# Kernel tuning notes

Hardware: AMD Instinct MI355X
Metric: run time of the kernel (lower is better)

The kernel has to match this reference:

```python
import jax, jax.numpy as jnp
import numpy as np

# bitsandbytes NF4 codebook (16 levels)
NF4 = jnp.array([-1.0, -0.6961928009986877, -0.5250730514526367, -0.39491748809814453,
                 -0.28444138169288635, -0.18477343022823334, -0.09105003625154495, 0.0,
                 0.07958029955625534, 0.16093020141124725, 0.24611230194568634,
                 0.33791524171829224, 0.44070982933044434, 0.5626170039176941,
                 0.7229568362236023, 1.0], dtype=jnp.float32)
BLOCK = 64  # NF4 quantization blocksize
HD, M, TOKENS = 4096, 11008, 512


def dequant_nf4(codes, absmax, out_f, in_f):
    # codes: int [out_f, in_f] in [0,16); absmax: float [out_f*in_f/BLOCK]
    w = NF4[codes.reshape(-1, BLOCK)] * absmax[:, None]
    return w.reshape(out_f, in_f)


def setup_inputs() -> dict:
    key = jax.random.key(0)
    ks = jax.random.split(key, 7)
    x = jax.random.normal(ks[0], (TOKENS, HD), dtype=jnp.float32)
    gate_codes = jax.random.randint(ks[1], (M, HD), 0, 16, dtype=jnp.int32)
    up_codes = jax.random.randint(ks[2], (M, HD), 0, 16, dtype=jnp.int32)
    down_codes = jax.random.randint(ks[3], (HD, M), 0, 16, dtype=jnp.int32)
    n_blk = (M * HD) // BLOCK
    gate_absmax = jax.random.uniform(ks[4], (n_blk,), dtype=jnp.float32) * 0.02 + 1e-3
    up_absmax = jax.random.uniform(ks[5], (n_blk,), dtype=jnp.float32) * 0.02 + 1e-3
    down_absmax = jax.random.uniform(ks[6], (n_blk,), dtype=jnp.float32) * 0.02 + 1e-3
    return {"x": x, "gate_codes": gate_codes, "gate_absmax": gate_absmax,
            "up_codes": up_codes, "up_absmax": up_absmax,
            "down_codes": down_codes, "down_absmax": down_absmax}


def reference(x, gate_codes, gate_absmax, up_codes, up_absmax, down_codes, down_absmax):
    # Dequantize NF4 weights on the fly, then SwiGLU MLP:
    # down( silu(gate(x)) * up(x) )
    Wg = dequant_nf4(gate_codes, gate_absmax, M, HD)   # [m, hd]
    Wu = dequant_nf4(up_codes, up_absmax, M, HD)       # [m, hd]
    Wd = dequant_nf4(down_codes, down_absmax, HD, M)   # [hd, m]
    g = x @ Wg.T                                       # [tokens, m]
    u = x @ Wu.T                                       # [tokens, m]
    h = jax.nn.silu(g) * u                             # [tokens, m]
    return h @ Wd.T                                    # [tokens, hd]
```

## Files before the change

kernel.cpp:

```cpp
#include <hip/hip_runtime.h>
#include <hip/hip_fp16.h>
#include <cstdint>
#include <cstddef>


using float4v = __attribute__((ext_vector_type(4))) float;
using half8   = __attribute__((ext_vector_type(8))) _Float16;

__constant__ float NF4TAB[16] = {
  -1.0f, -0.6961928009986877f, -0.5250730514526367f, -0.39491748809814453f,
  -0.28444138169288635f, -0.18477343022823334f, -0.09105003625154495f, 0.0f,
  0.07958029955625534f, 0.16093020141124725f, 0.24611230194568634f,
  0.33791524171829224f, 0.44070982933044434f, 0.5626170039176941f,
  0.7229568362236023f, 1.0f };

#define BARRIER() asm volatile("s_waitcnt lgkmcnt(0)\n\ts_barrier" ::: "memory")


template <bool ATOMIC>
__global__ __launch_bounds__(256, 3) void gemm_nf4(
    const __half* __restrict__ Apk,
    const int* __restrict__ c0, const float* __restrict__ am0,
    const int* __restrict__ c1, const float* __restrict__ am1,
    __half* __restrict__ o0, __half* __restrict__ o1,
    float* __restrict__ outF,
    int N, int K, int Kc, int Ntiles)
{
  __shared__ __half    Bb[2][32 * 80];
  __shared__ unsigned  ptab[256];

  const int tid  = threadIdx.x;
  const int lane = tid & 63;
  const int wave = tid >> 6;
  const int l15  = lane & 15;
  const int hi8  = (lane >> 4) << 3;

  {
    __half2 pr = __floats2half2_rn(NF4TAB[tid & 15], NF4TAB[tid >> 4]);
    ptab[tid] = *(const unsigned*)&pr;
  }

  int nt, r2;
  if (ATOMIC) {
    const int xcd  = blockIdx.x & 7;
    const int slot = blockIdx.x >> 3;
    r2 = xcd >> 1;
    nt = (xcd & 1) * (Ntiles >> 1) + slot;
  } else {
    const int nwg = gridDim.x;
    const int bid = (blockIdx.x & 7) * (nwg >> 3) + (blockIdx.x >> 3);
    nt = bid % Ntiles;
    r2 = bid / Ntiles;
  }

  const int k0 = ATOMIC ? r2 * Kc : 0;
  const int nk = Kc >> 6;
  const int* codes  = (!ATOMIC && r2) ? c1 : c0;
  const float* amax = (!ATOMIC && r2) ? am1 : am0;
  __half* outH      = (!ATOMIC && r2) ? o1 : o0;

  const int col0 = nt * 32;
  const int Kb   = K >> 6;

  const int bn = tid >> 3;
  const int bq = tid & 7;
  const int4* cSrc   = (const int4*)(codes + (size_t)(col0 + bn) * K + k0);
  const float* amSrc = amax + (size_t)(col0 + bn) * Kb + (k0 >> 6);

  const int kb0 = k0 >> 5;
  const int mb0 = wave * 8;
  const __half* pA = Apk + (size_t)mb0 * 512 + (size_t)lane * 8;

  float4v acc[8][2];
  {
    float4v z = {0.f, 0.f, 0.f, 0.f};
    #pragma unroll
    for (int i = 0; i < 8; ++i)
      #pragma unroll
      for (int j = 0; j < 2; ++j) acc[i][j] = z;
  }

  int4  cr[2][2];
  float amr[2];
  half8 apf[8], apf2[8];

#define LOADC(S, KT)                                                            \
  { const int4* _p = cSrc + (KT) * 16;                                          \
    cr[S][0] = _p[bq * 2]; cr[S][1] = _p[bq * 2 + 1];                           \
    amr[S] = amSrc[KT]; }

#define DEQB(BUFI, S)                                                           \
  { const __half _ah = __float2half(amr[S]);                                    \
    const __half2 _am2 = __half2{_ah, _ah};                                     \
    unsigned _w0 = ptab[cr[S][0].x | (cr[S][0].y << 4)];                        \
    unsigned _w1 = ptab[cr[S][0].z | (cr[S][0].w << 4)];                        \
    unsigned _w2 = ptab[cr[S][1].x | (cr[S][1].y << 4)];                        \
    unsigned _w3 = ptab[cr[S][1].z | (cr[S][1].w << 4)];                        \
    __half2 _p0 = __hmul2(*(const __half2*)&_w0, _am2);                         \
    __half2 _p1 = __hmul2(*(const __half2*)&_w1, _am2);                         \
    __half2 _p2 = __hmul2(*(const __half2*)&_w2, _am2);                         \
    __half2 _p3 = __hmul2(*(const __half2*)&_w3, _am2);                         \
    uint4 _wv;                                                                  \
    _wv.x = *(const unsigned*)&_p0; _wv.y = *(const unsigned*)&_p1;             \
    _wv.z = *(const unsigned*)&_p2; _wv.w = *(const unsigned*)&_p3;             \
    *(uint4*)&Bb[BUFI][bn * 80 + bq * 8] = _wv; }

#define LOADA(DST, KT, KK)                                                      \
  { const __half* _pa = pA + ((size_t)(kb0 + (KT) * 2 + (KK)) << 14);           \
    _Pragma("unroll")                                                           \
    for (int _i = 0; _i < 8; ++_i)                                              \
      DST[_i] = *(const half8*)(_pa + _i * 512); }

#define LDBF(BF, S, KK)                                                         \
  { _Pragma("unroll")                                                           \
    for (int _j = 0; _j < 2; ++_j)                                              \
      BF[_j] = *(const half8*)&Bb[S][(_j * 16 + l15) * 80 + (KK) * 32 + hi8]; }

#define MFMA16(APF, BF)                                                         \
  { _Pragma("unroll")                                                           \
    for (int _i = 0; _i < 8; ++_i)                                              \
      _Pragma("unroll")                                                         \
      for (int _j = 0; _j < 2; ++_j)                                            \
        acc[_i][_j] = __builtin_amdgcn_mfma_f32_16x16x32_f16(APF[_i], BF[_j], acc[_i][_j], 0, 0, 0); }

  LOADC(0, 0);
  if (nk > 1) LOADC(1, 1);
  BARRIER();
  DEQB(0, 0);
  if (nk > 2) LOADC(0, 2);
  BARRIER();

#define BODY(KT, S, NP)                                                         \
  { LOADA(apf, KT, 0);                                                          \
    if ((KT) + 1 < nk) DEQB(NP, NP);                                            \
    LOADA(apf2, KT, 1);                                                         \
    if ((KT) + 3 < nk) LOADC(NP, (KT) + 3);                                     \
    half8 bf[2];                                                                \
    LDBF(bf, S, 0);                                                             \
    MFMA16(apf, bf);                                                            \
    LDBF(bf, S, 1);                                                             \
    MFMA16(apf2, bf);                                                           \
    BARRIER(); }

  int kt = 0;
  while (kt + 2 <= nk) { BODY(kt, 0, 1); BODY(kt + 1, 1, 0); kt += 2; }
  if (kt < nk) BODY(kt, 0, 1);

  if (ATOMIC) {
    const int ccol0 = col0 + l15;
    const int crow0 = wave * 128 + ((lane >> 4) << 2);
    #pragma unroll
    for (int i = 0; i < 8; ++i)
      #pragma unroll
      for (int j = 0; j < 2; ++j)
        #pragma unroll
        for (int rr = 0; rr < 4; ++rr) {
          const size_t idx = (size_t)(crow0 + i * 16 + rr) * N + (ccol0 + j * 16);
          atomicAdd(&outF[idx], acc[i][j][rr]);
        }
  } else {
    const int jj    = lane & 7;
    const int lb    = (lane >> 3) & 1;
    const int rbase = (lane >> 4) << 2;
    const int kb    = col0 >> 5;
    #pragma unroll
    for (int i = 0; i < 8; ++i) {
      const int mb = wave * 8 + i;
      #pragma unroll
      for (int j = 0; j < 2; ++j) {
        const int lp = (j * 2 + lb) * 16 + rbase;
        #pragma unroll
        for (int rr = 0; rr < 4; ++rr) {
          const size_t a = ((size_t)(kb * 32 + mb) * 64 + (lp + rr)) * 8 + jj;
          outH[a] = __float2half(acc[i][j][rr]);
        }
      }
    }
  }
#undef LOADC
#undef DEQB
#undef LOADA
#undef LDBF
#undef MFMA16
#undef BODY
}

__global__ void cast_pack_kernel(const float* __restrict__ x,
                                 __half* __restrict__ xp, int nGrp) {
  int pid = blockIdx.x * blockDim.x + threadIdx.x;
  if (pid >= nGrp) return;
  const int lane = pid & 63;
  const int grp  = pid >> 6;
  const int mb   = grp & 31;
  const int kb   = grp >> 5;
  const int m = mb * 16 + (lane & 15);
  const int k = kb * 32 + ((lane >> 4) << 3);
  const float4* src = (const float4*)(x + (size_t)m * 4096 + k);
  float4 v0 = src[0], v1 = src[1];
  __half2 h0 = __floats2half2_rn(v0.x, v0.y), h1 = __floats2half2_rn(v0.z, v0.w);
  __half2 h2 = __floats2half2_rn(v1.x, v1.y), h3 = __floats2half2_rn(v1.z, v1.w);
  uint4 o;
  o.x = *(const unsigned*)&h0; o.y = *(const unsigned*)&h1;
  o.z = *(const unsigned*)&h2; o.w = *(const unsigned*)&h3;
  ((uint4*)xp)[pid] = o;
}

__global__ void swiglu_kernel(const __half* __restrict__ g,
                              const __half* __restrict__ u,
                              __half* __restrict__ h, int n2) {
  int i = blockIdx.x * blockDim.x + threadIdx.x;
  if (i < n2) {
    float2 gf = __half22float2(((const __half2*)g)[i]);
    float2 uf = __half22float2(((const __half2*)u)[i]);
    float h0 = gf.x / (1.f + __expf(-gf.x)) * uf.x;
    float h1 = gf.y / (1.f + __expf(-gf.y)) * uf.y;
    ((__half2*)h)[i] = __floats2half2_rn(h0, h1);
  }
}

extern "C" void kernel_launch(void* const* d_in, const int* in_sizes, int n_in,
                              void* d_out, int out_size, void* d_ws, size_t ws_size,
                              hipStream_t stream)
{
  (void)in_sizes; (void)n_in; (void)ws_size;
  const float* x            = (const float*)d_in[0];
  const int*   gate_codes   = (const int*)d_in[1];
  const float* gate_absmax  = (const float*)d_in[2];
  const int*   up_codes     = (const int*)d_in[3];
  const float* up_absmax    = (const float*)d_in[4];
  const int*   down_codes   = (const int*)d_in[5];
  const float* down_absmax  = (const float*)d_in[6];
  float* out = (float*)d_out;

  __half* xp = (__half*)d_ws;
  __half* g  = xp + (size_t)512 * 4096;
  __half* u  = g  + (size_t)512 * 11008;

  hipMemsetAsync(d_out, 0, (size_t)out_size * sizeof(float), stream);

  cast_pack_kernel<<<1024, 256, 0, stream>>>(x, xp, (512 * 4096) / 8);

  gemm_nf4<false><<<688, 256, 0, stream>>>(xp, gate_codes, gate_absmax,
                                           up_codes, up_absmax,
                                           g, u, nullptr,
                                           11008, 4096, 4096, 344);

  swiglu_kernel<<<11008, 256, 0, stream>>>(g, u, g, (512 * 11008) / 2);

  gemm_nf4<true><<<512, 256, 0, stream>>>(g, down_codes, down_absmax,
                                          nullptr, nullptr, nullptr, nullptr,
                                          out, 4096, 11008, 2752, 128);
}
```

Before: 684.3 us.

## Dequantize NF4 codes directly into MFMA B-fragments in registers, dropping LDS staging

Each lane now loads the int32 codes for its own MFMA B-fragment rows and dequantizes them straight into registers. This removes the shared-memory B tile, its double buffering, and the per-iteration barriers. The cost is redundant code loads across the four waves, since every wave reloads the same 32 columns of codes. Prefetch depth drops from two stages to one, with less explicit overlap between A loads and dequantization.

```diff
diff --git a/kernel.cpp b/kernel.cpp
--- a/kernel.cpp
+++ b/kernel.cpp
@@ -13,8 +13,6 @@
   0.07958029955625534f, 0.16093020141124725f, 0.24611230194568634f,
   0.33791524171829224f, 0.44070982933044434f, 0.5626170039176941f,
   0.7229568362236023f, 1.0f };
-
-#define BARRIER() asm volatile("s_waitcnt lgkmcnt(0)\n\ts_barrier" ::: "memory")
 
 
 template <bool ATOMIC>
@@ -26,8 +24,7 @@
     float* __restrict__ outF,
     int N, int K, int Kc, int Ntiles)
 {
-  __shared__ __half    Bb[2][32 * 80];
-  __shared__ unsigned  ptab[256];
+  __shared__ unsigned ptab[256];
 
   const int tid  = threadIdx.x;
   const int lane = tid & 63;
@@ -39,6 +36,7 @@
     __half2 pr = __floats2half2_rn(NF4TAB[tid & 15], NF4TAB[tid >> 4]);
     ptab[tid] = *(const unsigned*)&pr;
   }
+  __syncthreads();
 
   int nt, r2;
   if (ATOMIC) {
@@ -62,14 +60,14 @@
   const int col0 = nt * 32;
   const int Kb   = K >> 6;
 
-  const int bn = tid >> 3;
-  const int bq = tid & 7;
-  const int4* cSrc   = (const int4*)(codes + (size_t)(col0 + bn) * K + k0);
-  const float* amSrc = amax + (size_t)(col0 + bn) * Kb + (k0 >> 6);
-
-  const int kb0 = k0 >> 5;
-  const int mb0 = wave * 8;
-  const __half* pA = Apk + (size_t)mb0 * 512 + (size_t)lane * 8;
+  const int rowA = col0 + l15;
+  const int4*  c4a = (const int4*)(codes + (size_t)rowA * K + k0 + hi8);
+  const int4*  c4b = (const int4*)(codes + (size_t)(rowA + 16) * K + k0 + hi8);
+  const float* amA = amax + (size_t)rowA * Kb + (k0 >> 6);
+  const float* amB = amA + (size_t)16 * Kb;
+
+  const __half* pA = Apk + ((size_t)((k0 >> 5) * 32 + wave * 8)) * 512
+                         + (size_t)lane * 8;
 
   float4v acc[8][2];
   {
@@ -80,71 +78,66 @@
       for (int j = 0; j < 2; ++j) acc[i][j] = z;
   }
 
-  int4  cr[2][2];
-  float amr[2];
-  half8 apf[8], apf2[8];
-
-#define LOADC(S, KT)                                                            \
-  { const int4* _p = cSrc + (KT) * 16;                                          \
-    cr[S][0] = _p[bq * 2]; cr[S][1] = _p[bq * 2 + 1];                           \
-    amr[S] = amSrc[KT]; }
-
-#define DEQB(BUFI, S)                                                           \
-  { const __half _ah = __float2half(amr[S]);                                    \
-    const __half2 _am2 = __half2{_ah, _ah};                                     \
-    unsigned _w0 = ptab[cr[S][0].x | (cr[S][0].y << 4)];                        \
-    unsigned _w1 = ptab[cr[S][0].z | (cr[S][0].w << 4)];                        \
-    unsigned _w2 = ptab[cr[S][1].x | (cr[S][1].y << 4)];                        \
-    unsigned _w3 = ptab[cr[S][1].z | (cr[S][1].w << 4)];                        \
-    __half2 _p0 = __hmul2(*(const __half2*)&_w0, _am2);                         \
-    __half2 _p1 = __hmul2(*(const __half2*)&_w1, _am2);                         \
-    __half2 _p2 = __hmul2(*(const __half2*)&_w2, _am2);                         \
-    __half2 _p3 = __hmul2(*(const __half2*)&_w3, _am2);                         \
+  int4  cq[8];
+  float af[2];
+
+#define LOADCQ()                                                                \
+  { cq[0] = c4a[0]; cq[1] = c4a[1]; cq[2] = c4a[8]; cq[3] = c4a[9];             \
+    cq[4] = c4b[0]; cq[5] = c4b[1]; cq[6] = c4b[8]; cq[7] = c4b[9];             \
+    af[0] = *amA; af[1] = *amB;                                                 \
+    c4a += 16; c4b += 16; ++amA; ++amB; }
+
+#define DEQ1(DST, Q0, Q1, AM2)                                                  \
+  { unsigned _w0 = ptab[Q0.x | (Q0.y << 4)];                                    \
+    unsigned _w1 = ptab[Q0.z | (Q0.w << 4)];                                    \
+    unsigned _w2 = ptab[Q1.x | (Q1.y << 4)];                                    \
+    unsigned _w3 = ptab[Q1.z | (Q1.w << 4)];                                    \
+    __half2 _p0 = __hmul2(*(const __half2*)&_w0, AM2);                          \
+    __half2 _p1 = __hmul2(*(const __half2*)&_w1, AM2);                          \
+    __half2 _p2 = __hmul2(*(const __half2*)&_w2, AM2);                          \
+    __half2 _p3 = __hmul2(*(const __half2*)&_w3, AM2);                          \
     uint4 _wv;                                                                  \
     _wv.x = *(const unsigned*)&_p0; _wv.y = *(const unsigned*)&_p1;             \
     _wv.z = *(const unsigned*)&_p2; _wv.w = *(const unsigned*)&_p3;             \
-    *(uint4*)&Bb[BUFI][bn * 80 + bq * 8] = _wv; }
-
-#define LOADA(DST, KT, KK)                                                      \
-  { const __half* _pa = pA + ((size_t)(kb0 + (KT) * 2 + (KK)) << 14);           \
-    _Pragma("unroll")                                                           \
-    for (int _i = 0; _i < 8; ++_i)                                              \
-      DST[_i] = *(const half8*)(_pa + _i * 512); }
-
-#define LDBF(BF, S, KK)                                                         \
-  { _Pragma("unroll")                                                           \
-    for (int _j = 0; _j < 2; ++_j)                                              \
-      BF[_j] = *(const half8*)&Bb[S][(_j * 16 + l15) * 80 + (KK) * 32 + hi8]; }
-
-#define MFMA16(APF, BF)                                                         \
-  { _Pragma("unroll")                                                           \
-    for (int _i = 0; _i < 8; ++_i)                                              \
-      _Pragma("unroll")                                                         \
-      for (int _j = 0; _j < 2; ++_j)                                            \
-        acc[_i][_j] = __builtin_amdgcn_mfma_f32_16x16x32_f16(APF[_i], BF[_j], acc[_i][_j], 0, 0, 0); }
-
-  LOADC(0, 0);
-  if (nk > 1) LOADC(1, 1);
-  BARRIER();
-  DEQB(0, 0);
-  if (nk > 2) LOADC(0, 2);
-  BARRIER();
-
-#define BODY(KT, S, NP)                                                         \
-  { LOADA(apf, KT, 0);                                                          \
-    if ((KT) + 1 < nk) DEQB(NP, NP);                                            \
-    LOADA(apf2, KT, 1);                                                         \
-    if ((KT) + 3 < nk) LOADC(NP, (KT) + 3);                                     \
-    half8 bf[2];                                                                \
-    LDBF(bf, S, 0);                                                             \
-    MFMA16(apf, bf);                                                            \
-    LDBF(bf, S, 1);                                                             \
-    MFMA16(apf2, bf);                                                           \
-    BARRIER(); }
-
-  int kt = 0;
-  while (kt + 2 <= nk) { BODY(kt, 0, 1); BODY(kt + 1, 1, 0); kt += 2; }
-  if (kt < nk) BODY(kt, 0, 1);
+    DST = *(const half8*)&_wv; }
+
+  LOADCQ();
+
+  for (int kt = 0; kt < nk; ++kt) {
+    const __half _a0 = __float2half(af[0]);
+    const __half _a1 = __float2half(af[1]);
+    const __half2 am20{_a0, _a0}, am21{_a1, _a1};
+    half8 bq00, bq01, bq10, bq11;
+    DEQ1(bq00, cq[0], cq[1], am20);
+    DEQ1(bq01, cq[2], cq[3], am20);
+    DEQ1(bq10, cq[4], cq[5], am21);
+    DEQ1(bq11, cq[6], cq[7], am21);
+
+    half8 ap[8];
+    #pragma unroll
+    for (int i = 0; i < 8; ++i)
+      ap[i] = *(const half8*)(pA + i * 512);
+
+    if (kt + 1 < nk) LOADCQ();
+
+    #pragma unroll
+    for (int i = 0; i < 8; ++i) {
+      acc[i][0] = __builtin_amdgcn_mfma_f32_16x16x32_f16(ap[i], bq00, acc[i][0], 0, 0, 0);
+      acc[i][1] = __builtin_amdgcn_mfma_f32_16x16x32_f16(ap[i], bq10, acc[i][1], 0, 0, 0);
+    }
+
+    #pragma unroll
+    for (int i = 0; i < 8; ++i)
+      ap[i] = *(const half8*)(pA + 16384 + i * 512);
+
+    #pragma unroll
+    for (int i = 0; i < 8; ++i) {
+      acc[i][0] = __builtin_amdgcn_mfma_f32_16x16x32_f16(ap[i], bq01, acc[i][0], 0, 0, 0);
+      acc[i][1] = __builtin_amdgcn_mfma_f32_16x16x32_f16(ap[i], bq11, acc[i][1], 0, 0, 0);
+    }
+
+    pA += 32768;
+  }
 
   if (ATOMIC) {
     const int ccol0 = col0 + l15;
@@ -177,12 +170,8 @@
       }
     }
   }
-#undef LOADC
-#undef DEQB
-#undef LOADA
-#undef LDBF
-#undef MFMA16
-#undef BODY
+#undef LOADCQ
+#undef DEQ1
 }
 
 __global__ void cast_pack_kernel(const float* __restrict__ x,
```

After: 890.5 us. 1.3x slower.
